# Kernel optimization log

Hardware: AMD Instinct MI355X
Metric: run time of the kernel (lower is better)

## Reference

```python
import jax, jax.numpy as jnp
import numpy as np

B, S_LEN, H_LEN, DIM = 2048, 64, 256, 256
NULL_ATT = -float(2 ** 22)


def setup_inputs() -> dict:
    key = jax.random.key(0)
    k1, k2, k3, k4, k5, k6, k7 = jax.random.split(key, 7)
    return {
        "item_emb": jax.random.normal(k1, (B, DIM), dtype=jnp.float32),
        "x_session": jax.random.normal(k2, (B, S_LEN, DIM), dtype=jnp.float32),
        "session_len": jax.random.randint(k3, (B,), 0, S_LEN, dtype=jnp.int32),
        "user_hist": jax.random.normal(k4, (B, H_LEN, DIM), dtype=jnp.float32),
        "hist_len": jax.random.randint(k5, (B,), 0, H_LEN, dtype=jnp.int32),
        "W1": jax.random.normal(k6, (DIM, 2 * DIM), dtype=jnp.float32) * 0.05,
        "b1": jax.random.normal(k7, (DIM,), dtype=jnp.float32) * 0.05,
    }


def reference(item_emb, x_session, session_len, user_hist, hist_len, W1, b1):
    # item_emb [B,d], x_session [B,s,d], user_hist [B,h,d]
    batch, s_len, dim = x_session.shape
    h_len = user_hist.shape[1]
    # fc1 query does not depend on history position -> compute once per (b,s)
    q_in = jnp.concatenate(
        [jnp.broadcast_to(item_emb[:, None, :], x_session.shape), x_session], axis=-1
    )  # [B,s,2d]
    query = q_in @ W1.T + b1  # [B,s,d]
    # attention scores: sum over dim of hist * query for every (s,h) pair
    att = jnp.einsum("bsd,bhd->bsh", query, user_hist)  # [B,s,h]
    mask_s = (jnp.arange(s_len)[None, :] < session_len[:, None])[:, :, None]
    mask_h = (jnp.arange(h_len)[None, :] < hist_len[:, None])[:, None, :]
    att = jnp.where(mask_s & mask_h, att, jnp.float32(NULL_ATT))
    score = jnp.max(att, axis=1)  # max over session positions -> [B,h]
    w = jax.nn.softmax(score, axis=1)  # [B,h]
    user_hist_rep = jnp.sum(user_hist * w[:, :, None], axis=1)  # [B,d]
    return user_hist_rep, score
```

## Files before the change

### kernel.cpp

```cpp
#include <hip/hip_runtime.h>

#define NB 2048
#define NULL_ATT (-4194304.0f)

typedef __attribute__((ext_vector_type(8))) _Float16 f16x8;
typedef __attribute__((ext_vector_type(2))) _Float16 h2;
typedef __attribute__((ext_vector_type(4))) float f32x4;

__device__ __align__(16) short g_wxf16[256 * 256];
__device__ float g_iq[NB * 256];

__device__ __forceinline__ int qoff(int s, int k) {
    int g = k >> 3;
    return s * 256 + (((g ^ (s & 7)) << 3) | (k & 7));
}

__device__ __forceinline__ f16x8 cvt8h(float4 a, float4 b) {
    f16x8 r;
    r[0] = (_Float16)a.x; r[1] = (_Float16)a.y; r[2] = (_Float16)a.z; r[3] = (_Float16)a.w;
    r[4] = (_Float16)b.x; r[5] = (_Float16)b.y; r[6] = (_Float16)b.z; r[7] = (_Float16)b.w;
    return r;
}

__device__ __forceinline__ void stage8(const float* __restrict__ p, f16x8 dst[8]) {
    float4 r[8][2];
    #pragma unroll
    for (int kc = 0; kc < 8; ++kc) {
        r[kc][0] = *(const float4*)(p + kc * 32);
        r[kc][1] = *(const float4*)(p + kc * 32 + 4);
    }
    #pragma unroll
    for (int kc = 0; kc < 8; ++kc) dst[kc] = cvt8h(r[kc][0], r[kc][1]);
}

__global__ void conv_w1(const float* __restrict__ W1) {
    int j = blockIdx.x, k = threadIdx.x;
    g_wxf16[j * 256 + k] = __builtin_bit_cast(short, (_Float16)W1[(size_t)j * 512 + 256 + k]);
}

__global__ __launch_bounds__(256, 4) void iq_gemm(const float* __restrict__ item_emb,
                                                  const float* __restrict__ W1,
                                                  const float* __restrict__ b1) {
    const int m0 = blockIdx.x * 16;
    const int t = threadIdx.x, wave = t >> 6, lane = t & 63;
    const int lr = lane & 15, lo8 = lane >> 4;
    const int jb = wave * 64;

    f16x8 afr[8];
    stage8(item_emb + (size_t)(m0 + lr) * 256 + lo8 * 8, afr);

    f32x4 acc[4];
    #pragma unroll
    for (int jt = 0; jt < 4; ++jt) acc[jt] = f32x4{0.f, 0.f, 0.f, 0.f};
    #pragma unroll
    for (int kc = 0; kc < 8; ++kc) {
        #pragma unroll
        for (int jt = 0; jt < 4; ++jt) {
            const float* wp = W1 + (size_t)(jb + jt * 16 + lr) * 512 + kc * 32 + lo8 * 8;
            f16x8 bfr = cvt8h(*(const float4*)wp, *(const float4*)(wp + 4));
            acc[jt] = __builtin_amdgcn_mfma_f32_16x16x32_f16(afr[kc], bfr, acc[jt], 0, 0, 0);
        }
    }
    #pragma unroll
    for (int jt = 0; jt < 4; ++jt) {
        float bv = b1[jb + jt * 16 + lr];
        #pragma unroll
        for (int i = 0; i < 4; ++i)
            g_iq[(size_t)(m0 + lo8 * 4 + i) * 256 + jb + jt * 16 + lr] = acc[jt][i] + bv;
    }
}

#define AA_GET(i) (h2{bcur[(i) >> 2][(((i) & 3) << 1)], bcur[(i) >> 2][(((i) & 3) << 1) | 1]})
#define AA_SET(i, v) { bcur[(i) >> 2][(((i) & 3) << 1)] = (v)[0]; \
                       bcur[(i) >> 2][(((i) & 3) << 1) | 1] = (v)[1]; }

__global__ __launch_bounds__(256, 4) void coatt_main(
    const float* __restrict__ x_session,
    const int*   __restrict__ session_len,
    const float* __restrict__ user_hist,
    const int*   __restrict__ hist_len,
    float* __restrict__ out)
{
    const int b = blockIdx.x;
    const int t = threadIdx.x;
    const int wave = t >> 6;
    const int lane = t & 63;
    const int lr  = lane & 15;
    const int lo8 = lane >> 4;
    const int sl = session_len[b];
    const int hl = hist_len[b];

    __shared__ __align__(16) short qf[64 * 256];
    __shared__ float sMax[256];
    __shared__ float red2[8];
    __shared__ __align__(16) float Vp[4][256];

    sMax[t] = NULL_ATT;
    const int nst = (sl > 0) ? min(4, (sl + 15) >> 4) : 0;

    if (wave < nst) {
        const int st = wave;
        f16x8 afr[8];
        stage8(x_session + ((size_t)b * 64 + st * 16 + lr) * 256 + lo8 * 8, afr);

        #pragma unroll
        for (int jc = 0; jc < 4; ++jc) {
            f32x4 acc[4];
            #pragma unroll
            for (int jt = 0; jt < 4; ++jt) {
                float v = g_iq[(size_t)b * 256 + jc * 64 + jt * 16 + lr];
                acc[jt] = f32x4{v, v, v, v};
            }
            #pragma unroll
            for (int kc = 0; kc < 8; ++kc) {
                #pragma unroll
                for (int jt = 0; jt < 4; ++jt) {
                    f16x8 bfr2 = *(const f16x8*)&g_wxf16[(jc * 64 + jt * 16 + lr) * 256 + kc * 32 + lo8 * 8];
                    acc[jt] = __builtin_amdgcn_mfma_f32_16x16x32_f16(afr[kc], bfr2, acc[jt], 0, 0, 0);
                }
            }
            #pragma unroll
            for (int jt = 0; jt < 4; ++jt) {
                int j = jc * 64 + jt * 16 + lr;
                #pragma unroll
                for (int i = 0; i < 4; ++i)
                    qf[qoff(st * 16 + lo8 * 4 + i, j)] =
                        __builtin_bit_cast(short, (_Float16)acc[jt][i]);
            }
        }
    }

    const int nht = (hl + 15) >> 4;
    const bool p2 = (nst > 0 && hl > 0);
    const float* hB = user_hist + (size_t)b * 256 * 256;
    f16x8 bcur[8];
    if (p2 && wave < nht)
        stage8(hB + (size_t)(wave * 16 + lr) * 256 + lo8 * 8, bcur);
    __syncthreads();

    float Mrun = -3.0e38f;
    float Drun = 0.0f;
    float Vr0 = 0.f, Vr1 = 0.f, Vr2 = 0.f, Vr3 = 0.f;
    if (p2) {
        for (int slot = 0; slot < 4; ++slot) {
            const int ht = wave + slot * 4;
            if (ht >= nht) break;
            if (slot > 0)
                stage8(hB + (size_t)(ht * 16 + lr) * 256 + lo8 * 8, bcur);

            f32x4 acc[4];
            #pragma unroll
            for (int st = 0; st < 4; ++st) acc[st] = f32x4{0.f, 0.f, 0.f, 0.f};
            #pragma unroll
            for (int kc = 0; kc < 8; ++kc) {
                #pragma unroll
                for (int st = 0; st < 4; ++st) {
                    if (st < nst) {
                        f16x8 a = *(const f16x8*)&qf[qoff(st * 16 + lr, kc * 32 + lo8 * 8)];
                        acc[st] = __builtin_amdgcn_mfma_f32_16x16x32_f16(a, bcur[kc], acc[st], 0, 0, 0);
                    }
                }
            }
            float m = NULL_ATT;
            #pragma unroll
            for (int st = 0; st < 4; ++st) {
                if (st < nst) {
                    #pragma unroll
                    for (int i = 0; i < 4; ++i) {
                        int s = st * 16 + lo8 * 4 + i;
                        if (s < sl) m = fmaxf(m, acc[st][i]);
                    }
                }
            }
            m = fmaxf(m, __shfl_xor(m, 16, 64));
            m = fmaxf(m, __shfl_xor(m, 32, 64));
            const int h = ht * 16 + lr;
            if (lane < 16 && h < hl) sMax[h] = m;

            float sh = (h < hl) ? m : NULL_ATT;
            float mt = sh;
            mt = fmaxf(mt, __shfl_xor(mt, 1, 64));
            mt = fmaxf(mt, __shfl_xor(mt, 2, 64));
            mt = fmaxf(mt, __shfl_xor(mt, 4, 64));
            mt = fmaxf(mt, __shfl_xor(mt, 8, 64));
            float mnew = fmaxf(Mrun, mt);
            float scl = __expf(Mrun - mnew);
            Vr0 *= scl; Vr1 *= scl; Vr2 *= scl; Vr3 *= scl;
            Drun *= scl;
            Mrun = mnew;
            float eh = __expf(sh - Mrun);
            Drun += eh;

            {
                const _Float16 e16 = (_Float16)eh;
                f16x8 e8 = {e16, e16, e16, e16, e16, e16, e16, e16};
                #pragma unroll
                for (int kc = 0; kc < 8; ++kc) bcur[kc] *= e8;
            }
            #pragma unroll
            for (int sb = 0; sb < 4; ++sb) {
                const int bmask = 8 >> sb;
                const int half = 16 >> sb;
                const bool hi = (lr & bmask) != 0;
                #pragma unroll
                for (int i = 0; i < (16 >> sb); ++i) {
                    h2 a0 = AA_GET(i);
                    h2 a1 = AA_GET(i + half);
                    h2 keep = hi ? a1 : a0;
                    h2 send = hi ? a0 : a1;
                    int ru = __shfl_xor(__builtin_bit_cast(int, send), bmask, 64);
                    h2 res = keep + __builtin_bit_cast(h2, ru);
                    AA_SET(i, res);
                }
            }
            h2 f0 = AA_GET(0), f1 = AA_GET(1);
            Vr0 += (float)f0[0];
            Vr1 += (float)f0[1];
            Vr2 += (float)f1[0];
            Vr3 += (float)f1[1];
        }
        float Dl = Drun;
        Dl += __shfl_xor(Dl, 1, 64);
        Dl += __shfl_xor(Dl, 2, 64);
        Dl += __shfl_xor(Dl, 4, 64);
        Dl += __shfl_xor(Dl, 8, 64);
        if (lane == 0) { red2[wave] = Mrun; red2[4 + wave] = Dl; }
        const int col0 = (lr >> 1) * 32 + lo8 * 8 + (lr & 1) * 4;
        *(float4*)&Vp[wave][col0] = float4{Vr0, Vr1, Vr2, Vr3};
    }
    __syncthreads();

    float sc = sMax[t];
    out[(size_t)NB * 256 + (size_t)b * 256 + t] = sc;

    if (p2) {
        float M0 = red2[0], M1 = red2[1], M2 = red2[2], M3 = red2[3];
        float Ms = fmaxf(fmaxf(M0, M1), fmaxf(M2, M3));
        float w0 = __expf(M0 - Ms), w1 = __expf(M1 - Ms);
        float w2 = __expf(M2 - Ms), w3 = __expf(M3 - Ms);
        float denom = w0 * red2[4] + w1 * red2[5] + w2 * red2[6] + w3 * red2[7];
        float num = w0 * Vp[0][t] + w1 * Vp[1][t] + w2 * Vp[2][t] + w3 * Vp[3][t];
        out[(size_t)b * 256 + t] = num / denom;
    } else {
        f32x4 a4 = {0.f, 0.f, 0.f, 0.f};
        const float* hc = hB + lane * 4;
        for (int h = wave; h < 256; h += 16) {
            float4 v0 = *(const float4*)(hc + (size_t)(h)      * 256);
            float4 v1 = *(const float4*)(hc + (size_t)(h + 4)  * 256);
            float4 v2 = *(const float4*)(hc + (size_t)(h + 8)  * 256);
            float4 v3 = *(const float4*)(hc + (size_t)(h + 12) * 256);
            a4[0] += (v0.x + v1.x) + (v2.x + v3.x);
            a4[1] += (v0.y + v1.y) + (v2.y + v3.y);
            a4[2] += (v0.z + v1.z) + (v2.z + v3.z);
            a4[3] += (v0.w + v1.w) + (v2.w + v3.w);
        }
        *(float4*)&Vp[wave][lane * 4] = float4{a4[0], a4[1], a4[2], a4[3]};
        __syncthreads();
        out[(size_t)b * 256 + t] =
            ((Vp[0][t] + Vp[1][t]) + (Vp[2][t] + Vp[3][t])) * (1.0f / 256.0f);
    }
}

extern "C" void kernel_launch(void* const* d_in, const int* in_sizes, int n_in,
                              void* d_out, int out_size, void* d_ws, size_t ws_size,
                              hipStream_t stream) {
    const float* item_emb    = (const float*)d_in[0];
    const float* x_session   = (const float*)d_in[1];
    const int*   session_len = (const int*)d_in[2];
    const float* user_hist   = (const float*)d_in[3];
    const int*   hist_len    = (const int*)d_in[4];
    const float* W1          = (const float*)d_in[5];
    const float* b1          = (const float*)d_in[6];
    float* out = (float*)d_out;

    conv_w1<<<256, 256, 0, stream>>>(W1);
    iq_gemm<<<128, 256, 0, stream>>>(item_emb, W1, b1);
    coatt_main<<<NB, 256, 0, stream>>>(x_session, session_len, user_hist, hist_len, out);
}
```

Measured before the change: 178.6 us.

## Merge prep kernels and defer cross-lane history reduction until after all slots

Merges the W1 fp16 conversion kernel and the item-query GEMM into one launch, with block index selecting the role, which removes one kernel launch. In the attention loop, the per-slot butterfly shuffle reduction of the softmax-weighted history is replaced by accumulating into a per-lane fp16 array (parr), with a single shuffle reduction after all slots. The rescale on a max change is now conditional. This cuts shuffle traffic per tile but accumulates in fp16 across slots and uses more registers, which risks precision loss and lower occupancy.

```diff
diff --git a/kernel.cpp b/kernel.cpp
--- a/kernel.cpp
+++ b/kernel.cpp
@@ -33,15 +33,16 @@
     for (int kc = 0; kc < 8; ++kc) dst[kc] = cvt8h(r[kc][0], r[kc][1]);
 }
 
-__global__ void conv_w1(const float* __restrict__ W1) {
-    int j = blockIdx.x, k = threadIdx.x;
-    g_wxf16[j * 256 + k] = __builtin_bit_cast(short, (_Float16)W1[(size_t)j * 512 + 256 + k]);
-}
-
-__global__ __launch_bounds__(256, 4) void iq_gemm(const float* __restrict__ item_emb,
-                                                  const float* __restrict__ W1,
-                                                  const float* __restrict__ b1) {
-    const int m0 = blockIdx.x * 16;
+__global__ __launch_bounds__(256, 4) void prep(const float* __restrict__ item_emb,
+                                               const float* __restrict__ W1,
+                                               const float* __restrict__ b1) {
+    if (blockIdx.x < 256) {
+        int j = blockIdx.x, k = threadIdx.x;
+        g_wxf16[j * 256 + k] =
+            __builtin_bit_cast(short, (_Float16)W1[(size_t)j * 512 + 256 + k]);
+        return;
+    }
+    const int m0 = (blockIdx.x - 256) * 16;
     const int t = threadIdx.x, wave = t >> 6, lane = t & 63;
     const int lr = lane & 15, lo8 = lane >> 4;
     const int jb = wave * 64;
@@ -70,9 +71,9 @@
     }
 }
 
-#define AA_GET(i) (h2{bcur[(i) >> 2][(((i) & 3) << 1)], bcur[(i) >> 2][(((i) & 3) << 1) | 1]})
-#define AA_SET(i, v) { bcur[(i) >> 2][(((i) & 3) << 1)] = (v)[0]; \
-                       bcur[(i) >> 2][(((i) & 3) << 1) | 1] = (v)[1]; }
+#define AA_GET(i) (h2{parr[(i) >> 2][(((i) & 3) << 1)], parr[(i) >> 2][(((i) & 3) << 1) | 1]})
+#define AA_SET(i, v) { parr[(i) >> 2][(((i) & 3) << 1)] = (v)[0]; \
+                       parr[(i) >> 2][(((i) & 3) << 1) | 1] = (v)[1]; }
 
 __global__ __launch_bounds__(256, 4) void coatt_main(
     const float* __restrict__ x_session,
@@ -140,7 +141,10 @@
 
     float Mrun = -3.0e38f;
     float Drun = 0.0f;
-    float Vr0 = 0.f, Vr1 = 0.f, Vr2 = 0.f, Vr3 = 0.f;
+    f16x8 parr[8];
+    #pragma unroll
+    for (int kc = 0; kc < 8; ++kc) parr[kc] = f16x8{0, 0, 0, 0, 0, 0, 0, 0};
+
     if (p2) {
         for (int slot = 0; slot < 4; ++slot) {
             const int ht = wave + slot * 4;
@@ -183,11 +187,15 @@
             mt = fmaxf(mt, __shfl_xor(mt, 2, 64));
             mt = fmaxf(mt, __shfl_xor(mt, 4, 64));
             mt = fmaxf(mt, __shfl_xor(mt, 8, 64));
-            float mnew = fmaxf(Mrun, mt);
-            float scl = __expf(Mrun - mnew);
-            Vr0 *= scl; Vr1 *= scl; Vr2 *= scl; Vr3 *= scl;
-            Drun *= scl;
-            Mrun = mnew;
+            if (mt > Mrun) {
+                float scl = __expf(Mrun - mt);
+                Drun *= scl;
+                const _Float16 s16 = (_Float16)scl;
+                f16x8 s8 = {s16, s16, s16, s16, s16, s16, s16, s16};
+                #pragma unroll
+                for (int kc = 0; kc < 8; ++kc) parr[kc] *= s8;
+                Mrun = mt;
+            }
             float eh = __expf(sh - Mrun);
             Drun += eh;
 
@@ -195,30 +203,28 @@
                 const _Float16 e16 = (_Float16)eh;
                 f16x8 e8 = {e16, e16, e16, e16, e16, e16, e16, e16};
                 #pragma unroll
-                for (int kc = 0; kc < 8; ++kc) bcur[kc] *= e8;
-            }
-            #pragma unroll
-            for (int sb = 0; sb < 4; ++sb) {
-                const int bmask = 8 >> sb;
-                const int half = 16 >> sb;
-                const bool hi = (lr & bmask) != 0;
-                #pragma unroll
-                for (int i = 0; i < (16 >> sb); ++i) {
-                    h2 a0 = AA_GET(i);
-                    h2 a1 = AA_GET(i + half);
-                    h2 keep = hi ? a1 : a0;
-                    h2 send = hi ? a0 : a1;
-                    int ru = __shfl_xor(__builtin_bit_cast(int, send), bmask, 64);
-                    h2 res = keep + __builtin_bit_cast(h2, ru);
-                    AA_SET(i, res);
-                }
-            }
-            h2 f0 = AA_GET(0), f1 = AA_GET(1);
-            Vr0 += (float)f0[0];
-            Vr1 += (float)f0[1];
-            Vr2 += (float)f1[0];
-            Vr3 += (float)f1[1];
-        }
+                for (int kc = 0; kc < 8; ++kc) parr[kc] = bcur[kc] * e8 + parr[kc];
+            }
+        }
+
+        #pragma unroll
+        for (int sb = 0; sb < 4; ++sb) {
+            const int bmask = 8 >> sb;
+            const int half = 16 >> sb;
+            const bool hi = (lr & bmask) != 0;
+            #pragma unroll
+            for (int i = 0; i < (16 >> sb); ++i) {
+                h2 a0 = AA_GET(i);
+                h2 a1 = AA_GET(i + half);
+                h2 keep = hi ? a1 : a0;
+                h2 send = hi ? a0 : a1;
+                int ru = __shfl_xor(__builtin_bit_cast(int, send), bmask, 64);
+                h2 res = keep + __builtin_bit_cast(h2, ru);
+                AA_SET(i, res);
+            }
+        }
+        h2 f0 = AA_GET(0), f1 = AA_GET(1);
+
         float Dl = Drun;
         Dl += __shfl_xor(Dl, 1, 64);
         Dl += __shfl_xor(Dl, 2, 64);
@@ -226,7 +232,8 @@
         Dl += __shfl_xor(Dl, 8, 64);
         if (lane == 0) { red2[wave] = Mrun; red2[4 + wave] = Dl; }
         const int col0 = (lr >> 1) * 32 + lo8 * 8 + (lr & 1) * 4;
-        *(float4*)&Vp[wave][col0] = float4{Vr0, Vr1, Vr2, Vr3};
+        *(float4*)&Vp[wave][col0] =
+            float4{(float)f0[0], (float)f0[1], (float)f1[0], (float)f1[1]};
     }
     __syncthreads();
 
@@ -273,7 +280,6 @@
     const float* b1          = (const float*)d_in[6];
     float* out = (float*)d_out;
 
-    conv_w1<<<256, 256, 0, stream>>>(W1);
-    iq_gemm<<<128, 256, 0, stream>>>(item_emb, W1, b1);
+    prep<<<384, 256, 0, stream>>>(item_emb, W1, b1);
     coatt_main<<<NB, 256, 0, stream>>>(x_session, session_len, user_hist, hist_len, out);
 }
```

New measurement: 181.3 us. Within noise of the previous version (+1.5%).

## Merge prep kernels and alias reduction buffers onto query LDS

Applied to the files above, without the earlier changes.

Combines the W1 conversion and item-query GEMM into one launch of 384 blocks, saving one kernel launch. In the main kernel, the score/max scratch arrays are removed: scores are written straight to global output, and the partial-V and reduction buffers reuse the query fp16 LDS region after an extra barrier. This cuts LDS per block, which may help occupancy, at the cost of extra barriers and scattered global score writes. The score output is pre-filled with NULL_ATT and then overwritten, which adds a redundant store per element.

```diff
diff --git a/kernel.cpp b/kernel.cpp
--- a/kernel.cpp
+++ b/kernel.cpp
@@ -33,15 +33,16 @@
     for (int kc = 0; kc < 8; ++kc) dst[kc] = cvt8h(r[kc][0], r[kc][1]);
 }
 
-__global__ void conv_w1(const float* __restrict__ W1) {
-    int j = blockIdx.x, k = threadIdx.x;
-    g_wxf16[j * 256 + k] = __builtin_bit_cast(short, (_Float16)W1[(size_t)j * 512 + 256 + k]);
-}
-
-__global__ __launch_bounds__(256, 4) void iq_gemm(const float* __restrict__ item_emb,
-                                                  const float* __restrict__ W1,
-                                                  const float* __restrict__ b1) {
-    const int m0 = blockIdx.x * 16;
+__global__ __launch_bounds__(256, 2) void prep(const float* __restrict__ item_emb,
+                                               const float* __restrict__ W1,
+                                               const float* __restrict__ b1) {
+    if (blockIdx.x < 256) {
+        int j = blockIdx.x, k = threadIdx.x;
+        g_wxf16[j * 256 + k] =
+            __builtin_bit_cast(short, (_Float16)W1[(size_t)j * 512 + 256 + k]);
+        return;
+    }
+    const int m0 = (blockIdx.x - 256) * 16;
     const int t = threadIdx.x, wave = t >> 6, lane = t & 63;
     const int lr = lane & 15, lo8 = lane >> 4;
     const int jb = wave * 64;
@@ -91,12 +92,16 @@
     const int hl = hist_len[b];
 
     __shared__ __align__(16) short qf[64 * 256];
-    __shared__ float sMax[256];
-    __shared__ float red2[8];
-    __shared__ __align__(16) float Vp[4][256];
-
-    sMax[t] = NULL_ATT;
+    float* VpA   = (float*)qf;
+    float* red2A = (float*)qf + 1024;
+
+    out[(size_t)NB * 256 + (size_t)b * 256 + t] = NULL_ATT;
+
     const int nst = (sl > 0) ? min(4, (sl + 15) >> 4) : 0;
+    const int nht = (hl + 15) >> 4;
+    const bool p2 = (nst > 0 && hl > 0);
+    const float* hB = user_hist + (size_t)b * 256 * 256;
+    float* scoreOut = out + (size_t)NB * 256 + (size_t)b * 256;
 
     if (wave < nst) {
         const int st = wave;
@@ -130,9 +135,6 @@
         }
     }
 
-    const int nht = (hl + 15) >> 4;
-    const bool p2 = (nst > 0 && hl > 0);
-    const float* hB = user_hist + (size_t)b * 256 * 256;
     f16x8 bcur[8];
     if (p2 && wave < nht)
         stage8(hB + (size_t)(wave * 16 + lr) * 256 + lo8 * 8, bcur);
@@ -175,7 +177,7 @@
             m = fmaxf(m, __shfl_xor(m, 16, 64));
             m = fmaxf(m, __shfl_xor(m, 32, 64));
             const int h = ht * 16 + lr;
-            if (lane < 16 && h < hl) sMax[h] = m;
+            if (lane < 16 && h < hl) scoreOut[h] = m;
 
             float sh = (h < hl) ? m : NULL_ATT;
             float mt = sh;
@@ -224,22 +226,19 @@
         Dl += __shfl_xor(Dl, 2, 64);
         Dl += __shfl_xor(Dl, 4, 64);
         Dl += __shfl_xor(Dl, 8, 64);
-        if (lane == 0) { red2[wave] = Mrun; red2[4 + wave] = Dl; }
+
+        __syncthreads();
+        if (lane == 0) { red2A[wave] = Mrun; red2A[4 + wave] = Dl; }
         const int col0 = (lr >> 1) * 32 + lo8 * 8 + (lr & 1) * 4;
-        *(float4*)&Vp[wave][col0] = float4{Vr0, Vr1, Vr2, Vr3};
-    }
-    __syncthreads();
-
-    float sc = sMax[t];
-    out[(size_t)NB * 256 + (size_t)b * 256 + t] = sc;
-
-    if (p2) {
-        float M0 = red2[0], M1 = red2[1], M2 = red2[2], M3 = red2[3];
+        *(float4*)&VpA[wave * 256 + col0] = float4{Vr0, Vr1, Vr2, Vr3};
+        __syncthreads();
+
+        float M0 = red2A[0], M1 = red2A[1], M2 = red2A[2], M3 = red2A[3];
         float Ms = fmaxf(fmaxf(M0, M1), fmaxf(M2, M3));
         float w0 = __expf(M0 - Ms), w1 = __expf(M1 - Ms);
         float w2 = __expf(M2 - Ms), w3 = __expf(M3 - Ms);
-        float denom = w0 * red2[4] + w1 * red2[5] + w2 * red2[6] + w3 * red2[7];
-        float num = w0 * Vp[0][t] + w1 * Vp[1][t] + w2 * Vp[2][t] + w3 * Vp[3][t];
+        float denom = w0 * red2A[4] + w1 * red2A[5] + w2 * red2A[6] + w3 * red2A[7];
+        float num = w0 * VpA[t] + w1 * VpA[256 + t] + w2 * VpA[512 + t] + w3 * VpA[768 + t];
         out[(size_t)b * 256 + t] = num / denom;
     } else {
         f32x4 a4 = {0.f, 0.f, 0.f, 0.f};
@@ -254,10 +253,11 @@
             a4[2] += (v0.z + v1.z) + (v2.z + v3.z);
             a4[3] += (v0.w + v1.w) + (v2.w + v3.w);
         }
-        *(float4*)&Vp[wave][lane * 4] = float4{a4[0], a4[1], a4[2], a4[3]};
+        __syncthreads();
+        *(float4*)&VpA[wave * 256 + lane * 4] = float4{a4[0], a4[1], a4[2], a4[3]};
         __syncthreads();
         out[(size_t)b * 256 + t] =
-            ((Vp[0][t] + Vp[1][t]) + (Vp[2][t] + Vp[3][t])) * (1.0f / 256.0f);
+            ((VpA[t] + VpA[256 + t]) + (VpA[512 + t] + VpA[768 + t])) * (1.0f / 256.0f);
     }
 }
 
@@ -273,7 +273,6 @@
     const float* b1          = (const float*)d_in[6];
     float* out = (float*)d_out;
 
-    conv_w1<<<256, 256, 0, stream>>>(W1);
-    iq_gemm<<<128, 256, 0, stream>>>(item_emb, W1, b1);
+    prep<<<384, 256, 0, stream>>>(item_emb, W1, b1);
     coatt_main<<<NB, 256, 0, stream>>>(x_session, session_len, user_hist, hist_len, out);
 }
```

New measurement: 186.0 us. 4.2% more time.
